# Performance work log

Hardware: AMD Instinct MI355X
Metric: run time of the kernel (lower is better)

Reference implementation:

```python
import jax, jax.numpy as jnp
import numpy as np

B, T, D, H = 4, 2048, 1024, 16
Hd = D // H


def setup_inputs() -> dict:
    key = jax.random.key(0)
    ks = jax.random.split(key, 6)
    s = 1.0 / np.sqrt(D)
    return {
        "x": jax.random.normal(ks[0], (B, T, D), dtype=jnp.float32),
        "mask": jnp.zeros((B, T), dtype=bool),
        "Wq": jax.random.normal(ks[1], (D, D), dtype=jnp.float32) * s,
        "bq": jnp.zeros((D,), dtype=jnp.float32),
        "Wk": jax.random.normal(ks[2], (D, D), dtype=jnp.float32) * s,
        "bk": jnp.zeros((D,), dtype=jnp.float32),
        "Wv": jax.random.normal(ks[3], (D, D), dtype=jnp.float32) * s,
        "bv": jnp.zeros((D,), dtype=jnp.float32),
        "Wo": jax.random.normal(ks[4], (D, D), dtype=jnp.float32) * s,
        "bo": jnp.zeros((D,), dtype=jnp.float32),
    }


def reference(x, mask, Wq, bq, Wk, bk, Wv, bv, Wo, bo):
    b, t, d = x.shape
    # projections -> [B, T, H, Hd]
    Q = (x @ Wq + bq).reshape(b, t, H, Hd)
    K = (x @ Wk + bk).reshape(b, t, H, Hd)
    V = (x @ Wv + bv).reshape(b, t, H, Hd)
    scale = jnp.asarray(Hd, x.dtype) ** -0.5
    # full score matrix [B, H, Tq, Tk] (matches the naive torch impl)
    attn = jnp.einsum("bqhd,bkhd->bhqk", Q, K) * scale
    attn = jnp.where(mask[:, None, None, :], jnp.asarray(-1e9, attn.dtype), attn)
    attn = jax.nn.softmax(attn, axis=-1)
    out = jnp.einsum("bhqk,bkhd->bqhd", attn, V).reshape(b, t, d)
    return out @ Wo + bo
```

## Files before the change

### kernel.cpp

```cpp
#include <hip/hip_runtime.h>

using bf16 = __bf16;
typedef bf16 bf16x4 __attribute__((ext_vector_type(4)));
typedef bf16 bf16x8 __attribute__((ext_vector_type(8)));
typedef float f32x4 __attribute__((ext_vector_type(4)));
typedef float f32x8 __attribute__((ext_vector_type(8)));

#define MFMA16(a, b, c) __builtin_amdgcn_mfma_f32_16x16x32_bf16(a, b, c, 0, 0, 0)

constexpr int Bb = 4, Tt = 2048, Dd = 1024, Hh = 16, Hd = 64;
constexpr int Mrows = Bb * Tt;
constexpr float CEXP = 0.18033688011112042f;

__device__ __forceinline__ void gload_lds16(const bf16* g, bf16* lds_base) {
  __builtin_amdgcn_global_load_lds((const __attribute__((address_space(1))) void*)g,
                                   (__attribute__((address_space(3))) void*)lds_base,
                                   16, 0, 0);
}

__global__ void cast_f32_bf16_kernel(const float* __restrict__ in, bf16* __restrict__ out) {
  size_t i = ((size_t)blockIdx.x * 256 + threadIdx.x) * 8;
  f32x8 v = *(const f32x8*)(in + i);
  *(bf16x8*)(out + i) = __builtin_convertvector(v, bf16x8);
}

__global__ void transpose_cast_w4_kernel(const float* __restrict__ Wq, const float* __restrict__ Wk,
                                         const float* __restrict__ Wv, const float* __restrict__ Wo,
                                         bf16* __restrict__ Wt, bf16* __restrict__ Wot) {
  __shared__ alignas(16) float tile[64][68];
  const int tid = threadIdx.x;
  const int n0 = blockIdx.x * 64, k0 = blockIdx.y * 64, z = blockIdx.z;
  const float* W = (z == 0) ? Wq : (z == 1) ? Wk : (z == 2) ? Wv : Wo;
  bf16* dst = (z == 3) ? Wot : (Wt + (size_t)z * Dd * Dd);
  const float scale = (z == 0) ? CEXP : 1.0f;
#pragma unroll
  for (int it = 0; it < 4; ++it) {
    int chunk = tid + it * 256;
    int kr = chunk >> 4, c4 = chunk & 15;
    f32x4 v = *(const f32x4*)(W + (size_t)(k0 + kr) * Dd + n0 + c4 * 4);
    *(f32x4*)&tile[kr][c4 * 4] = v * scale;
  }
  __syncthreads();
#pragma unroll
  for (int it = 0; it < 2; ++it) {
    int chunk = tid + it * 256;
    int n = chunk & 63, k8 = chunk >> 6;
    bf16x8 o;
#pragma unroll
    for (int j = 0; j < 8; ++j) o[j] = (bf16)tile[k8 * 8 + j][n];
    *(bf16x8*)(dst + (size_t)(n0 + n) * Dd + k0 + k8 * 8) = o;
  }
}

__global__ void pack_bias_kernel(const float* __restrict__ bq, const float* __restrict__ bk,
                                 const float* __restrict__ bv, float* __restrict__ outb) {
  int i = blockIdx.x * 256 + threadIdx.x;
  float v = (i < 1024) ? bq[i] * CEXP : (i < 2048 ? bk[i - 1024] : bv[i - 2048]);
  outb[i] = v;
}

constexpr int QBM = 128, QBN = 256, QBK = 32, QNT = Dd / QBK;

#define VMW(n) asm volatile("s_waitcnt vmcnt(" #n ")" ::: "memory")

__global__ __launch_bounds__(512, 2)
void gemm_qkv_kernel(const bf16* __restrict__ A, const bf16* __restrict__ Bt,
                     const float* __restrict__ bias, bf16* __restrict__ QK,
                     bf16* __restrict__ Vt) {
  constexpr int KD = Dd;
  __shared__ alignas(16) bf16 As[3][QBM * QBK];
  __shared__ alignas(16) bf16 Bs[3][QBN * QBK];
  const int tid = threadIdx.x;
  const int lane = tid & 63, wave = tid >> 6;
  const int col = lane & 15, quad = lane >> 4;
  const int wr = wave >> 2, wc = wave & 3;
  const size_t m0 = (size_t)blockIdx.x * QBM, n0 = (size_t)blockIdx.y * QBN;

  const int u = (lane & 7) ^ (lane >> 3);
  const int srow = 2 * (lane >> 3) + (u >> 2);
  const int scol = (u & 3) * 8;
  const bf16* Abase = A + (m0 + srow) * (size_t)KD + scol;
  const bf16* Bbase = Bt + (n0 + srow) * (size_t)KD + scol;

  const int pswz = (((col & 1) << 2) | quad) ^ (col >> 1);
  const int afb = wr * 2048 + (col >> 1) * 64 + pswz * 8;
  const int bfb = wc * 2048 + (col >> 1) * 64 + pswz * 8;

  f32x4 acc[4][4];
#pragma unroll
  for (int i = 0; i < 4; ++i)
#pragma unroll
    for (int j = 0; j < 4; ++j)
#pragma unroll
      for (int r = 0; r < 4; ++r) acc[i][j][r] = 0.f;

#define QSTAGE(t, sl) do { \
    gload_lds16(Abase + (size_t)(t) * QBK + (size_t)(wave * 16) * KD, &As[sl][wave * 512]); \
    gload_lds16(Bbase + (size_t)(t) * QBK + (size_t)(2 * wave) * 16 * KD, &Bs[sl][(2 * wave) * 512]); \
    gload_lds16(Bbase + (size_t)(t) * QBK + (size_t)(2 * wave + 1) * 16 * KD, &Bs[sl][(2 * wave + 1) * 512]); \
  } while (0)

#define QKV_TILE(cur, DOSTAGE, VM) do { \
    bf16x8 af[4], bfv[4]; \
    _Pragma("unroll") for (int j = 0; j < 4; ++j) bfv[j] = *(const bf16x8*)&Bs[cur][bfb + j * 512]; \
    _Pragma("unroll") for (int i = 0; i < 4; ++i) af[i] = *(const bf16x8*)&As[cur][afb + i * 512]; \
    DOSTAGE; \
    asm volatile("s_waitcnt lgkmcnt(0)" ::: "memory"); \
    __builtin_amdgcn_s_setprio(1); \
    _Pragma("unroll") for (int i = 0; i < 4; ++i) \
      _Pragma("unroll") for (int j = 0; j < 4; ++j) acc[i][j] = MFMA16(af[i], bfv[j], acc[i][j]); \
    __builtin_amdgcn_s_setprio(0); \
    VM; \
    __builtin_amdgcn_s_barrier(); \
  } while (0)

  QSTAGE(0, 0);
  QSTAGE(1, 1);
  VMW(3);
  __builtin_amdgcn_s_barrier();

#pragma unroll 1
  for (int t = 0; t < QNT - 2; t += 3) {
    QKV_TILE(0, QSTAGE(t + 2, 2), VMW(3));
    QKV_TILE(1, QSTAGE(t + 3, 0), VMW(3));
    QKV_TILE(2, QSTAGE(t + 4, 1), VMW(3));
  }
  QKV_TILE(0, (void)0, VMW(0));
  QKV_TILE(1, (void)0, (void)0);

  if (n0 < 2048) {
#pragma unroll
    for (int i = 0; i < 4; ++i)
#pragma unroll
      for (int j = 0; j < 4; ++j) {
        size_t row = m0 + wr * 64 + i * 16 + quad * 4;
        size_t c = n0 + wc * 64 + j * 16 + col;
        float bv = bias[c];
#pragma unroll
        for (int r = 0; r < 4; ++r) QK[(row + r) * 2048 + c] = (bf16)(acc[i][j][r] + bv);
      }
  } else {
#pragma unroll
    for (int i = 0; i < 4; ++i)
#pragma unroll
      for (int j = 0; j < 4; ++j) {
        size_t row = m0 + wr * 64 + i * 16 + quad * 4;
        int c = (int)(n0 + wc * 64 + j * 16 + col);
        float bv = bias[c];
        int dall = c - 2048, hh = dall >> 6, dd = dall & 63;
        int bi = (int)(row >> 11), trow = (int)(row & 2047);
        bf16x4 pk;
#pragma unroll
        for (int r = 0; r < 4; ++r) pk[r] = (bf16)(acc[i][j][r] + bv);
        *(bf16x4*)&Vt[((size_t)(bi * Hh + hh) * Hd + dd) * Tt + trow] = pk;
      }
  }
#undef QKV_TILE
#undef QSTAGE
}

__global__ __launch_bounds__(256)
void gemm_bf16_kernel(const bf16* __restrict__ A, const bf16* __restrict__ Bt,
                      const float* __restrict__ bias, float* __restrict__ C,
                      int M, int N, int K) {
  __shared__ alignas(16) bf16 As[128 * 64];
  __shared__ alignas(16) bf16 Bs[128 * 64];
  const int tid = threadIdx.x;
  const int lane = tid & 63, wave = tid >> 6;
  const int col = lane & 15, quad = lane >> 4;
  const int wr = (wave >> 1) * 64, wc = (wave & 1) * 64;
  const size_t m0 = (size_t)blockIdx.x * 128, n0 = (size_t)blockIdx.y * 128;
  const int srow = lane >> 3, schunk = (lane & 7) * 8;

  f32x4 acc[4][4];
#pragma unroll
  for (int i = 0; i < 4; ++i)
#pragma unroll
    for (int j = 0; j < 4; ++j)
#pragma unroll
      for (int r = 0; r < 4; ++r) acc[i][j][r] = 0.f;

  for (int k0 = 0; k0 < K; k0 += 64) {
#pragma unroll
    for (int it = 0; it < 4; ++it) {
      int rbase = it * 32 + wave * 8;
      gload_lds16(A + (m0 + rbase + srow) * (size_t)K + k0 + schunk, &As[rbase * 64]);
      gload_lds16(Bt + (n0 + rbase + srow) * (size_t)K + k0 + schunk, &Bs[rbase * 64]);
    }
    __syncthreads();
#pragma unroll
    for (int kk = 0; kk < 2; ++kk) {
      bf16x8 af[4], bfr[4];
#pragma unroll
      for (int i = 0; i < 4; ++i) af[i] = *(const bf16x8*)&As[(wr + i * 16 + col) * 64 + kk * 32 + quad * 8];
#pragma unroll
      for (int j = 0; j < 4; ++j) bfr[j] = *(const bf16x8*)&Bs[(wc + j * 16 + col) * 64 + kk * 32 + quad * 8];
#pragma unroll
      for (int i = 0; i < 4; ++i)
#pragma unroll
        for (int j = 0; j < 4; ++j) acc[i][j] = MFMA16(af[i], bfr[j], acc[i][j]);
    }
    __syncthreads();
  }
#pragma unroll
  for (int i = 0; i < 4; ++i)
#pragma unroll
    for (int j = 0; j < 4; ++j) {
      size_t row = m0 + wr + i * 16 + quad * 4;
      size_t c = n0 + wc + j * 16 + col;
      float bv = bias[c];
#pragma unroll
      for (int r = 0; r < 4; ++r) C[(row + r) * (size_t)N + c] = acc[i][j][r] + bv;
    }
}

__global__ __launch_bounds__(256, 2)
void flash_attn_kernel(const bf16* __restrict__ qk, const bf16* __restrict__ vt,
                       const unsigned char* __restrict__ mask, bf16* __restrict__ ao) {
  __shared__ alignas(16) bf16 Ks[3][64 * 64];
  __shared__ alignas(16) bf16 Vs[3][64 * 64];

  const int tid = threadIdx.x;
  const int wave = tid >> 6, lane = tid & 63;
  const int col = lane & 15, quad = lane >> 4;
  const int id = blockIdx.x;
  const int hb = id & 63, qi = id >> 6;
  const int h = hb & 15, b = hb >> 4;
  const int qbase0 = qi * 128 + wave * 32;

  const bf16* Qp = qk + (size_t)(b * Tt) * 2048 + h * Hd;
  const bf16* Kp = Qp + 1024;
  const bf16* Vp = vt + ((size_t)(b * Hh + h) * Hd) * Tt;
  const unsigned char* mp = mask + b * Tt;

  unsigned long long anym;
  {
    const unsigned long long* mq = (const unsigned long long*)mp;
    unsigned long long acc = 0;
#pragma unroll
    for (int j = 0; j < 4; ++j) acc |= mq[lane * 4 + j];
    anym = __ballot(acc != 0ull);
  }

  bf16x8 qf[2][2];
#pragma unroll
  for (int t = 0; t < 2; ++t)
#pragma unroll
    for (int kk = 0; kk < 2; ++kk)
      qf[t][kk] = *(const bf16x8*)(Qp + (size_t)(qbase0 + t * 16 + col) * 2048 + kk * 32 + quad * 8);

  const int u = (lane & 7) ^ (lane >> 3);
  const int g0 = 2 * wave, g1 = 2 * wave + 1;
  const bf16* Ksrc0 = Kp + (size_t)(g0 * 8 + (lane >> 3)) * 2048 + u * 8;
  const bf16* Ksrc1 = Kp + (size_t)(g1 * 8 + (lane >> 3)) * 2048 + u * 8;
  const bf16* Vsrc0 = Vp + (size_t)(g0 * 8 + (lane >> 3)) * 2048 + u * 8;
  const bf16* Vsrc1 = Vp + (size_t)(g1 * 8 + (lane >> 3)) * 2048 + u * 8;

#define FSTAGE(t, sl) do { \
    gload_lds16(Ksrc0 + (size_t)(t) * 64 * 2048, &Ks[sl][g0 * 512]); \
    gload_lds16(Ksrc1 + (size_t)(t) * 64 * 2048, &Ks[sl][g1 * 512]); \
    gload_lds16(Vsrc0 + (t) * 64, &Vs[sl][g0 * 512]); \
    gload_lds16(Vsrc1 + (t) * 64, &Vs[sl][g1 * 512]); \
  } while (0)

  f32x4 oacc[2][4];
  f32x4 lones[2];
#pragma unroll
  for (int t = 0; t < 2; ++t) {
#pragma unroll
    for (int r = 0; r < 4; ++r) lones[t][r] = 0.f;
#pragma unroll
    for (int n = 0; n < 4; ++n)
#pragma unroll
      for (int r = 0; r < 4; ++r) oacc[t][n][r] = 0.f;
  }
  const f32x4 zero4 = {0.f, 0.f, 0.f, 0.f};
  bf16x8 onev;
#pragma unroll
  for (int j = 0; j < 8; ++j) onev[j] = (bf16)1.0f;

  const int fslot0 = ((0 * 4 + quad) ^ (col & 7)) * 8;
  const int fslot1 = ((1 * 4 + quad) ^ (col & 7)) * 8;
  const int voff = (quad & 1) * 4;

#define FITER(cur, II, DOSTAGE, VM) do { \
    const int kb = (II) * 64; \
    DOSTAGE; \
    f32x4 s[2][4]; \
    _Pragma("unroll") for (int kt = 0; kt < 4; ++kt) { \
      bf16x8 kf0 = *(const bf16x8*)&Ks[cur][(kt * 16 + col) * 64 + fslot0]; \
      bf16x8 kf1 = *(const bf16x8*)&Ks[cur][(kt * 16 + col) * 64 + fslot1]; \
      s[0][kt] = MFMA16(kf0, qf[0][0], zero4); \
      s[1][kt] = MFMA16(kf0, qf[1][0], zero4); \
      s[0][kt] = MFMA16(kf1, qf[0][1], s[0][kt]); \
      s[1][kt] = MFMA16(kf1, qf[1][1], s[1][kt]); \
    } \
    if ((anym >> (2 * (II))) & 3ull) { \
      _Pragma("unroll") for (int kt = 0; kt < 4; ++kt) \
        _Pragma("unroll") for (int r = 0; r < 4; ++r) \
          if (mp[kb + kt * 16 + quad * 4 + r] != 0) { s[0][kt][r] = -1e9f; s[1][kt][r] = -1e9f; } \
    } \
    bf16x8 pf[2][2]; \
    _Pragma("unroll") for (int t = 0; t < 2; ++t) { \
      f32x4 e0, e1, e2, e3; \
      _Pragma("unroll") for (int r = 0; r < 4; ++r) { \
        e0[r] = __builtin_amdgcn_exp2f(s[t][0][r]); \
        e1[r] = __builtin_amdgcn_exp2f(s[t][1][r]); \
        e2[r] = __builtin_amdgcn_exp2f(s[t][2][r]); \
        e3[r] = __builtin_amdgcn_exp2f(s[t][3][r]); \
      } \
      bf16x4 c0 = __builtin_convertvector(e0, bf16x4); \
      bf16x4 c1 = __builtin_convertvector(e1, bf16x4); \
      bf16x4 c2 = __builtin_convertvector(e2, bf16x4); \
      bf16x4 c3 = __builtin_convertvector(e3, bf16x4); \
      pf[t][0] = __builtin_shufflevector(c0, c1, 0, 1, 2, 3, 4, 5, 6, 7); \
      pf[t][1] = __builtin_shufflevector(c2, c3, 0, 1, 2, 3, 4, 5, 6, 7); \
    } \
    _Pragma("unroll") for (int n = 0; n < 4; ++n) { \
      const int row = (n * 16 + col) * 64; \
      const int rx = col & 7; \
      bf16x8 v0, v1; \
      { bf16x4 lo = *(const bf16x4*)&Vs[cur][row + ((0 + (quad >> 1)) ^ rx) * 8 + voff]; \
        bf16x4 hi = *(const bf16x4*)&Vs[cur][row + ((2 + (quad >> 1)) ^ rx) * 8 + voff]; \
        v0 = __builtin_shufflevector(lo, hi, 0, 1, 2, 3, 4, 5, 6, 7); } \
      { bf16x4 lo = *(const bf16x4*)&Vs[cur][row + ((4 + (quad >> 1)) ^ rx) * 8 + voff]; \
        bf16x4 hi = *(const bf16x4*)&Vs[cur][row + ((6 + (quad >> 1)) ^ rx) * 8 + voff]; \
        v1 = __builtin_shufflevector(lo, hi, 0, 1, 2, 3, 4, 5, 6, 7); } \
      _Pragma("unroll") for (int t = 0; t < 2; ++t) { \
        oacc[t][n] = MFMA16(pf[t][0], v0, oacc[t][n]); \
        oacc[t][n] = MFMA16(pf[t][1], v1, oacc[t][n]); \
      } \
    } \
    _Pragma("unroll") for (int t = 0; t < 2; ++t) { \
      lones[t] = MFMA16(pf[t][0], onev, lones[t]); \
      lones[t] = MFMA16(pf[t][1], onev, lones[t]); \
    } \
    VM; \
    __builtin_amdgcn_s_barrier(); \
  } while (0)

  FSTAGE(0, 0);
  FSTAGE(1, 1);
  VMW(4);
  __builtin_amdgcn_s_barrier();

#pragma unroll 1
  for (int ii = 0; ii < 30; ii += 3) {
    FITER(0, ii + 0, FSTAGE(ii + 2, 2), VMW(4));
    FITER(1, ii + 1, FSTAGE(ii + 3, 0), VMW(4));
    FITER(2, ii + 2, FSTAGE(ii + 4, 1), VMW(4));
  }
  FITER(0, 30, (void)0, VMW(0));
  FITER(1, 31, (void)0, (void)0);

#undef FITER
#undef FSTAGE

#pragma unroll
  for (int t = 0; t < 2; ++t) {
    f32x4 rl;
#pragma unroll
    for (int r = 0; r < 4; ++r) rl[r] = __builtin_amdgcn_rcpf(lones[t][r]);
#pragma unroll
    for (int n = 0; n < 4; ++n)
#pragma unroll
      for (int r = 0; r < 4; ++r) {
        size_t q = (size_t)b * Tt + qbase0 + t * 16 + quad * 4 + r;
        ao[q * Dd + h * Hd + n * 16 + col] = (bf16)(oacc[t][n][r] * rl[r]);
      }
  }
}

extern "C" void kernel_launch(void* const* d_in, const int* in_sizes, int n_in,
                              void* d_out, int out_size, void* d_ws, size_t ws_size,
                              hipStream_t stream) {
  const float* x = (const float*)d_in[0];
  const unsigned char* mask = (const unsigned char*)d_in[1];
  const float* Wq = (const float*)d_in[2];
  const float* bq = (const float*)d_in[3];
  const float* Wk = (const float*)d_in[4];
  const float* bk = (const float*)d_in[5];
  const float* Wv = (const float*)d_in[6];
  const float* bv = (const float*)d_in[7];
  const float* Wo = (const float*)d_in[8];
  const float* bo = (const float*)d_in[9];
  float* out = (float*)d_out;

  char* ws = (char*)d_ws;
  size_t off = 0;
  auto alloc = [&](size_t bytes) {
    char* p = ws + off;
    off += (bytes + 255) & ~(size_t)255;
    return p;
  };
  bf16* xb  = (bf16*)alloc((size_t)Mrows * Dd * 2);
  bf16* Wt  = (bf16*)alloc((size_t)3 * Dd * Dd * 2);
  bf16* Wot = (bf16*)alloc((size_t)Dd * Dd * 2);
  bf16* QK  = (bf16*)alloc((size_t)Mrows * 2048 * 2);
  bf16* Vt  = (bf16*)alloc((size_t)Bb * Hh * Hd * Tt * 2);
  float* bqkv = (float*)alloc((size_t)3 * Dd * 4);

  cast_f32_bf16_kernel<<<Mrows * Dd / (256 * 8), 256, 0, stream>>>(x, xb);
  transpose_cast_w4_kernel<<<dim3(16, 16, 4), 256, 0, stream>>>(Wq, Wk, Wv, Wo, Wt, Wot);
  pack_bias_kernel<<<12, 256, 0, stream>>>(bq, bk, bv, bqkv);

  gemm_qkv_kernel<<<dim3(Mrows / QBM, 3 * Dd / QBN), 512, 0, stream>>>(
      xb, Wt, bqkv, QK, Vt);

  bf16* AO = xb;
  flash_attn_kernel<<<dim3(1024), 256, 0, stream>>>(QK, Vt, mask, AO);
  gemm_bf16_kernel<<<dim3(Mrows / 128, Dd / 128), 256, 0, stream>>>(
      AO, Wot, bo, out, Mrows, Dd, Dd);
}
```

Measured before the change: 286.3 us.

## Load V fragments directly from global memory into registers, bypassing LDS

V tiles are no longer staged through a triple-buffered LDS ring with async global-to-LDS loads. Each wave now reads its V MFMA operand fragments straight from global memory into registers at the start of every iteration, and the vmcnt waits are adjusted to cover only the K loads. This halves LDS use and drops the LDS reads for V, which could raise occupancy. The cost is that all four waves redundantly fetch the same V tile, using small 8-byte loads that are issued right before use with no prefetch distance, so global-load latency may be exposed.

```diff
diff --git a/kernel.cpp b/kernel.cpp
--- a/kernel.cpp
+++ b/kernel.cpp
@@ -218,7 +218,6 @@
 void flash_attn_kernel(const bf16* __restrict__ qk, const bf16* __restrict__ vt,
                        const unsigned char* __restrict__ mask, bf16* __restrict__ ao) {
   __shared__ alignas(16) bf16 Ks[3][64 * 64];
-  __shared__ alignas(16) bf16 Vs[3][64 * 64];
 
   const int tid = threadIdx.x;
   const int wave = tid >> 6, lane = tid & 63;
@@ -253,14 +252,11 @@
   const int g0 = 2 * wave, g1 = 2 * wave + 1;
   const bf16* Ksrc0 = Kp + (size_t)(g0 * 8 + (lane >> 3)) * 2048 + u * 8;
   const bf16* Ksrc1 = Kp + (size_t)(g1 * 8 + (lane >> 3)) * 2048 + u * 8;
-  const bf16* Vsrc0 = Vp + (size_t)(g0 * 8 + (lane >> 3)) * 2048 + u * 8;
-  const bf16* Vsrc1 = Vp + (size_t)(g1 * 8 + (lane >> 3)) * 2048 + u * 8;
-
-#define FSTAGE(t, sl) do { \
+  const bf16* Vrow = Vp + (size_t)col * Tt + quad * 4;
+
+#define KSTAGE(t, sl) do { \
     gload_lds16(Ksrc0 + (size_t)(t) * 64 * 2048, &Ks[sl][g0 * 512]); \
     gload_lds16(Ksrc1 + (size_t)(t) * 64 * 2048, &Ks[sl][g1 * 512]); \
-    gload_lds16(Vsrc0 + (t) * 64, &Vs[sl][g0 * 512]); \
-    gload_lds16(Vsrc1 + (t) * 64, &Vs[sl][g1 * 512]); \
   } while (0)
 
   f32x4 oacc[2][4];
@@ -281,10 +277,14 @@
 
   const int fslot0 = ((0 * 4 + quad) ^ (col & 7)) * 8;
   const int fslot1 = ((1 * 4 + quad) ^ (col & 7)) * 8;
-  const int voff = (quad & 1) * 4;
 
 #define FITER(cur, II, DOSTAGE, VM) do { \
     const int kb = (II) * 64; \
+    bf16x4 vv[4][2][2]; \
+    _Pragma("unroll") for (int n = 0; n < 4; ++n) \
+      _Pragma("unroll") for (int kk = 0; kk < 2; ++kk) \
+        _Pragma("unroll") for (int hf = 0; hf < 2; ++hf) \
+          vv[n][kk][hf] = *(const bf16x4*)(Vrow + (size_t)(n * 16) * Tt + kb + kk * 32 + hf * 16); \
     DOSTAGE; \
     f32x4 s[2][4]; \
     _Pragma("unroll") for (int kt = 0; kt < 4; ++kt) { \
@@ -317,15 +317,8 @@
       pf[t][1] = __builtin_shufflevector(c2, c3, 0, 1, 2, 3, 4, 5, 6, 7); \
     } \
     _Pragma("unroll") for (int n = 0; n < 4; ++n) { \
-      const int row = (n * 16 + col) * 64; \
-      const int rx = col & 7; \
-      bf16x8 v0, v1; \
-      { bf16x4 lo = *(const bf16x4*)&Vs[cur][row + ((0 + (quad >> 1)) ^ rx) * 8 + voff]; \
-        bf16x4 hi = *(const bf16x4*)&Vs[cur][row + ((2 + (quad >> 1)) ^ rx) * 8 + voff]; \
-        v0 = __builtin_shufflevector(lo, hi, 0, 1, 2, 3, 4, 5, 6, 7); } \
-      { bf16x4 lo = *(const bf16x4*)&Vs[cur][row + ((4 + (quad >> 1)) ^ rx) * 8 + voff]; \
-        bf16x4 hi = *(const bf16x4*)&Vs[cur][row + ((6 + (quad >> 1)) ^ rx) * 8 + voff]; \
-        v1 = __builtin_shufflevector(lo, hi, 0, 1, 2, 3, 4, 5, 6, 7); } \
+      bf16x8 v0 = __builtin_shufflevector(vv[n][0][0], vv[n][0][1], 0, 1, 2, 3, 4, 5, 6, 7); \
+      bf16x8 v1 = __builtin_shufflevector(vv[n][1][0], vv[n][1][1], 0, 1, 2, 3, 4, 5, 6, 7); \
       _Pragma("unroll") for (int t = 0; t < 2; ++t) { \
         oacc[t][n] = MFMA16(pf[t][0], v0, oacc[t][n]); \
         oacc[t][n] = MFMA16(pf[t][1], v1, oacc[t][n]); \
@@ -339,22 +332,22 @@
     __builtin_amdgcn_s_barrier(); \
   } while (0)
 
-  FSTAGE(0, 0);
-  FSTAGE(1, 1);
-  VMW(4);
+  KSTAGE(0, 0);
+  KSTAGE(1, 1);
+  VMW(2);
   __builtin_amdgcn_s_barrier();
 
 #pragma unroll 1
   for (int ii = 0; ii < 30; ii += 3) {
-    FITER(0, ii + 0, FSTAGE(ii + 2, 2), VMW(4));
-    FITER(1, ii + 1, FSTAGE(ii + 3, 0), VMW(4));
-    FITER(2, ii + 2, FSTAGE(ii + 4, 1), VMW(4));
+    FITER(0, ii + 0, KSTAGE(ii + 2, 2), VMW(2));
+    FITER(1, ii + 1, KSTAGE(ii + 3, 0), VMW(2));
+    FITER(2, ii + 2, KSTAGE(ii + 4, 1), VMW(2));
   }
   FITER(0, 30, (void)0, VMW(0));
   FITER(1, 31, (void)0, (void)0);
 
 #undef FITER
-#undef FSTAGE
+#undef KSTAGE
 
 #pragma unroll
   for (int t = 0; t < 2; ++t) {
```

After: 447.9 us. 1.56x slower.
